# Kernel tuning notes

Measured on AMD Instinct MI355X. Metric: run time of the kernel, lower is better.

The kernel has to match this reference:

```python
import math
import jax, jax.numpy as jnp
import numpy as np

PHI = (1.0 + math.sqrt(5.0)) / 2.0
B, S, E, H, L = 2, 2048, 1024, 16, 5
DH = E // H


def setup_inputs() -> dict:
    key = jax.random.key(0)
    ks = jax.random.split(key, 16)
    rn = lambda k, sh, sc=0.02: jax.random.normal(k, sh, jnp.float32) * sc
    return {
        'x': jax.random.normal(ks[0], (B, S, E), jnp.float32),
        'consciousness_levels': jax.random.uniform(ks[1], (B, H), jnp.float32),
        'Wc': rn(ks[2], (L, E, E)), 'bc': jnp.zeros((L, E), jnp.float32),
        'Wf': rn(ks[3], (L, E, H)), 'bf': jnp.zeros((L, H), jnp.float32),
        'Wq': rn(ks[4], (E, E)), 'bq': jnp.zeros((E,), jnp.float32),
        'Wk': rn(ks[5], (E, E)), 'bk': jnp.zeros((E,), jnp.float32),
        'Wv': rn(ks[6], (E, E)), 'bv': jnp.zeros((E,), jnp.float32),
        'Wo': rn(ks[7], (E, E)), 'bo': jnp.zeros((E,), jnp.float32),
        'Wc1': rn(ks[8], (2 * DH, E)), 'bc1': jnp.zeros((E,), jnp.float32),
        'Wc2': rn(ks[9], (E, 1)), 'bc2': jnp.zeros((1,), jnp.float32),
        'gate': jax.random.normal(ks[10], (L, H), jnp.float32) / math.sqrt(H),
        'phi_phase': PHI * jnp.arange(H, dtype=jnp.float32),
        'ln_g': jnp.ones((E,), jnp.float32), 'ln_b': jnp.zeros((E,), jnp.float32),
    }


def reference(x, consciousness_levels, Wc, bc, Wf, bf, Wq, bq, Wk, bk, Wv, bv,
              Wo, bo, Wc1, bc1, Wc2, bc2, gate, phi_phase, ln_g, ln_b):
    b, s, e = x.shape
    l, _, h = Wf.shape
    dh = e // h
    # per-level consciousness scalar: consciousness_levels[:, level % num_heads] -> [B, L]
    cl = consciousness_levels[:, jnp.arange(l) % h]
    # consciousness-enhanced features: mean over L of (x @ Wc_l + bc_l) * cl[:, l]
    feat = jnp.einsum('bse,leo->lbso', x, Wc) + bc[:, None, None, :]   # [L,B,S,E]
    ce = jnp.mean(feat * cl.T[:, :, None, None], axis=0)                # [B,S,E]
    # QKV projections (spectral_norm linears; normalized weights supplied directly)
    Q = (ce @ Wq + bq).reshape(b, s, h, dh).transpose(0, 2, 1, 3)       # [B,H,S,Dh]
    K = (ce @ Wk + bk).reshape(b, s, h, dh).transpose(0, 2, 1, 3)
    V = (ce @ Wv + bv).reshape(b, s, h, dh).transpose(0, 2, 1, 3)
    scores = jnp.einsum('bhsd,bhtd->bhst', Q, K) / math.sqrt(dh)        # [B,H,S,S]
    # phi-harmonic phase modulation (scalar per (B,H), averaged over levels)
    pooled = ce.mean(axis=1)                                            # [B,E]
    freq = jnp.einsum('be,leh->lbh', pooled, Wf) + bf[:, None, :]       # [L,B,H]
    phase = jnp.sin(phi_phase[None, None, :] * freq * cl.T[:, :, None]).mean(axis=0)  # [B,H]
    scores = scores + 0.1 * phase[:, :, None, None]
    # quantum coherence gate per (B,H): sigmoid MLP on pooled Q/K head features
    ci = jnp.concatenate([Q.mean(axis=2), K.mean(axis=2)], axis=-1)     # [B,H,2*Dh]
    cw = jax.nn.sigmoid(jax.nn.gelu(ci @ Wc1 + bc1, approximate=False) @ Wc2 + bc2)  # [B,H,1]
    scores = scores * (1.0 + cw[..., None])
    aw = jax.nn.softmax(scores, axis=-1)
    # consciousness gating on attention weights, then re-softmax
    gw = jax.nn.softmax(gate, axis=1)                                   # [L,H]
    factor = jnp.prod(1.0 + 0.1 * cl[:, :, None] * gw[None, :, :], axis=1)  # [B,H]
    aw = jax.nn.softmax(aw * factor[:, :, None, None], axis=-1)
    attended = jnp.einsum('bhst,bhtd->bhsd', aw, V)
    out = attended.transpose(0, 2, 1, 3).reshape(b, s, e) @ Wo + bo
    y = x + out  # dropout is identity in eval
    mu = y.mean(axis=-1, keepdims=True)
    var = ((y - mu) ** 2).mean(axis=-1, keepdims=True)
    return (y - mu) / jnp.sqrt(var + 1e-5) * ln_g + ln_b
```

## Files before the change

### kernel.cpp

```cpp
#include <hip/hip_runtime.h>
#include <math.h>

#define BB 2
#define SS 2048
#define EE 1024
#define HH 16
#define LL 5
#define DH 64
#define QS (3 * EE)

typedef __attribute__((ext_vector_type(8))) short bf16x8;
typedef __attribute__((ext_vector_type(4))) float f32x4;

__device__ __forceinline__ unsigned short f2bf(float f) {
  unsigned u = __float_as_uint(f);
  u += 0x7fffu + ((u >> 16) & 1u);
  return (unsigned short)(u >> 16);
}
__device__ __forceinline__ float bf2f(unsigned short u) {
  return __uint_as_float((unsigned)u << 16);
}
__device__ __forceinline__ f32x4 mfma16(bf16x8 a, bf16x8 b, f32x4 c) {
  return __builtin_amdgcn_mfma_f32_16x16x32_bf16(a, b, c, 0, 0, 0);
}
__device__ __forceinline__ unsigned cvtpk(float a, float b) {
  unsigned r;
  asm("v_cvt_pk_bf16_f32 %0, %1, %2" : "=v"(r) : "v"(a), "v"(b));
  return r;
}
__device__ __forceinline__ void gload16(const unsigned short* g, unsigned short* l) {
  __builtin_amdgcn_global_load_lds(
      (const __attribute__((address_space(1))) void*)g,
      (__attribute__((address_space(3))) void*)l, 16, 0, 0);
}

__global__ void prep_kernel(const float* __restrict__ cons,
                            const float* __restrict__ gate,
                            float* __restrict__ cl, float* __restrict__ factor) {
  if (threadIdx.x == 0 && blockIdx.x == 0) {
    float clv[BB][LL];
    for (int b = 0; b < BB; ++b)
      for (int l = 0; l < LL; ++l) {
        clv[b][l] = cons[b * HH + (l % HH)];
        cl[b * LL + l] = clv[b][l];
      }
    float gw[LL][HH];
    for (int l = 0; l < LL; ++l) {
      float mx = -1e30f;
      for (int h = 0; h < HH; ++h) mx = fmaxf(mx, gate[l * HH + h]);
      float s = 0.f;
      for (int h = 0; h < HH; ++h) { gw[l][h] = expf(gate[l * HH + h] - mx); s += gw[l][h]; }
      for (int h = 0; h < HH; ++h) gw[l][h] /= s;
    }
    for (int b = 0; b < BB; ++b)
      for (int h = 0; h < HH; ++h) {
        float f = 1.f;
        for (int l = 0; l < LL; ++l) f *= 1.f + 0.1f * clv[b][l] * gw[l][h];
        factor[b * HH + h] = f;
      }
  }
}

__global__ void small_pack(const float* __restrict__ bc, const float* __restrict__ cl,
                           const float* __restrict__ bq, const float* __restrict__ bk,
                           const float* __restrict__ bv,
                           float* __restrict__ beff, float* __restrict__ bqkv) {
  int i = blockIdx.x * 256 + threadIdx.x;
  if (i < BB * EE) {
    int b = i >> 10, e = i & 1023;
    float a = 0.f;
    #pragma unroll
    for (int l = 0; l < LL; ++l) a += cl[b * LL + l] * bc[l * EE + e];
    beff[i] = a * (1.f / LL);
  } else {
    int j = i - BB * EE;
    float v = (j < EE) ? bq[j] : (j < 2 * EE) ? bk[j - EE] : bv[j - 2 * EE];
    bqkv[j] = v;
  }
}

__global__ __launch_bounds__(256) void wceffT_kernel(const float* __restrict__ Wc,
                                                     const float* __restrict__ cl,
                                                     unsigned short* __restrict__ Wt) {
  int o0 = blockIdx.x * 64, e0 = blockIdx.y * 64, b = blockIdx.z;
  __shared__ float t[64][69];
  int tid = threadIdx.x;
  float w[LL];
  #pragma unroll
  for (int l = 0; l < LL; ++l) w[l] = cl[b * LL + l] * (1.f / LL);
  #pragma unroll
  for (int i = 0; i < 4; ++i) {
    int idx = tid + i * 256;
    int r = idx >> 4, c4 = idx & 15;
    float4 acc = {0.f, 0.f, 0.f, 0.f};
    #pragma unroll
    for (int l = 0; l < LL; ++l) {
      float4 v = *(const float4*)&Wc[(long)l * EE * EE + (long)(e0 + r) * EE + o0 + c4 * 4];
      acc.x += w[l] * v.x; acc.y += w[l] * v.y; acc.z += w[l] * v.z; acc.w += w[l] * v.w;
    }
    t[r][c4 * 4 + 0] = acc.x; t[r][c4 * 4 + 1] = acc.y;
    t[r][c4 * 4 + 2] = acc.z; t[r][c4 * 4 + 3] = acc.w;
  }
  __syncthreads();
  #pragma unroll
  for (int i = 0; i < 2; ++i) {
    int idx = tid + i * 256;
    int o = idx >> 3, ech = idx & 7;
    unsigned short u[8];
    #pragma unroll
    for (int j = 0; j < 8; ++j) u[j] = f2bf(t[ech * 8 + j][o]);
    unsigned short* dst = Wt + (long)b * EE * EE + (long)(o0 + o) * EE + e0 + ech * 8;
    *(ushort4*)&dst[0] = *(ushort4*)&u[0];
    *(ushort4*)&dst[4] = *(ushort4*)&u[4];
  }
}

__global__ __launch_bounds__(256) void wT4_kernel(
    const float* __restrict__ W0, const float* __restrict__ W1,
    const float* __restrict__ W2, const float* __restrict__ W3,
    unsigned short* __restrict__ Wqkvt, unsigned short* __restrict__ Wot) {
  int z = blockIdx.z;
  const float* W = (z == 0) ? W0 : (z == 1) ? W1 : (z == 2) ? W2 : W3;
  unsigned short* Wt = (z < 3) ? (Wqkvt + (size_t)z * EE * EE) : Wot;
  int o0 = blockIdx.x * 64, e0 = blockIdx.y * 64;
  __shared__ float t[64][69];
  int tid = threadIdx.x;
  #pragma unroll
  for (int i = 0; i < 4; ++i) {
    int idx = tid + i * 256;
    int r = idx >> 4, c4 = idx & 15;
    float4 v = *(const float4*)&W[(long)(e0 + r) * EE + o0 + c4 * 4];
    t[r][c4 * 4 + 0] = v.x; t[r][c4 * 4 + 1] = v.y;
    t[r][c4 * 4 + 2] = v.z; t[r][c4 * 4 + 3] = v.w;
  }
  __syncthreads();
  #pragma unroll
  for (int i = 0; i < 2; ++i) {
    int idx = tid + i * 256;
    int o = idx >> 3, ech = idx & 7;
    unsigned short u[8];
    #pragma unroll
    for (int j = 0; j < 8; ++j) u[j] = f2bf(t[ech * 8 + j][o]);
    unsigned short* dst = Wt + (long)(o0 + o) * EE + e0 + ech * 8;
    *(ushort4*)&dst[0] = *(ushort4*)&u[0];
    *(ushort4*)&dst[4] = *(ushort4*)&u[4];
  }
}

__global__ void cvt_bf_kernel(const float* __restrict__ in, unsigned short* __restrict__ out) {
  long i = (long)blockIdx.x * 256 + threadIdx.x;
  float4 a = ((const float4*)in)[i * 2];
  float4 b = ((const float4*)in)[i * 2 + 1];
  ushort4 u0 = make_ushort4(f2bf(a.x), f2bf(a.y), f2bf(a.z), f2bf(a.w));
  ushort4 u1 = make_ushort4(f2bf(b.x), f2bf(b.y), f2bf(b.z), f2bf(b.w));
  ((ushort4*)out)[i * 2] = u0;
  ((ushort4*)out)[i * 2 + 1] = u1;
}

template <int OUTBF>
__global__ __launch_bounds__(256) void gemm_bf(
    const unsigned short* __restrict__ A, const unsigned short* __restrict__ Bt,
    const float* __restrict__ bias, void* __restrict__ C,
    int N, int K, long As_z, long Ws_z, long Bs_z, long Cs_z) {
  int flat = blockIdx.x + gridDim.x * (blockIdx.y + gridDim.y * blockIdx.z);
  int nwg = gridDim.x * gridDim.y * gridDim.z;
  flat = (flat & 7) * (nwg >> 3) + (flat >> 3);
  int nt_ = flat % gridDim.x;
  int rest = flat / gridDim.x;
  int mt_ = rest % gridDim.y;
  int z = rest / gridDim.y;

  const unsigned short* Ab = A + z * As_z + (long)mt_ * 128 * K;
  const unsigned short* Bb = Bt + z * Ws_z + (long)nt_ * 64 * K;
  const float* bb = bias + z * Bs_z + nt_ * 64;

  __shared__ __align__(16) unsigned short As[2][128 * 64];
  __shared__ __align__(16) unsigned short Bs[2][64 * 64];
  int tid = threadIdx.x;
  int w = tid >> 6, lane = tid & 63, c = lane & 15, g = lane >> 4;
  int wrow = (w >> 1) * 64, wcol = (w & 1) * 32;

  #define STAGE_A(kt, buf)                                                     \
    {                                                                          \
      const unsigned short* s_ = Ab + (kt) * 64;                               \
      _Pragma("unroll") for (int j = 0; j < 4; ++j) {                          \
        int base = (w * 4 + j) * 64;                                           \
        int idx = base + lane;                                                 \
        int row = idx >> 3, ch = idx & 7;                                      \
        gload16(s_ + (long)row * K + ((ch ^ (row & 7)) << 3),                  \
                &As[buf][base * 8]);                                           \
      }                                                                        \
    }
  #define STAGE_B(kt, buf)                                                     \
    {                                                                          \
      const unsigned short* s_ = Bb + (kt) * 64;                               \
      _Pragma("unroll") for (int j = 0; j < 2; ++j) {                          \
        int base = (w * 2 + j) * 64;                                           \
        int idx = base + lane;                                                 \
        int row = idx >> 3, ch = idx & 7;                                      \
        gload16(s_ + (long)row * K + ((ch ^ (row & 7)) << 3),                  \
                &Bs[buf][base * 8]);                                           \
      }                                                                        \
    }

  f32x4 acc[4][2];
  #pragma unroll
  for (int mi = 0; mi < 4; ++mi)
    #pragma unroll
    for (int ni = 0; ni < 2; ++ni) acc[mi][ni] = {0.f, 0.f, 0.f, 0.f};

  int nk = K >> 6;
  STAGE_A(0, 0) STAGE_B(0, 0)
  __syncthreads();
  int buf = 0;
  for (int kt = 0; kt < nk; ++kt) {
    if (kt + 1 < nk) { STAGE_A(kt + 1, buf ^ 1) STAGE_B(kt + 1, buf ^ 1) }
    #pragma unroll
    for (int kk = 0; kk < 2; ++kk) {
      bf16x8 af[4], bfv[2];
      #pragma unroll
      for (int mi = 0; mi < 4; ++mi) {
        int row = wrow + mi * 16 + c;
        af[mi] = *(const bf16x8*)&As[buf][row * 64 + ((((kk << 2) + g) ^ (row & 7)) << 3)];
      }
      #pragma unroll
      for (int ni = 0; ni < 2; ++ni) {
        int row = wcol + ni * 16 + c;
        bfv[ni] = *(const bf16x8*)&Bs[buf][row * 64 + ((((kk << 2) + g) ^ (row & 7)) << 3)];
      }
      #pragma unroll
      for (int mi = 0; mi < 4; ++mi)
        #pragma unroll
        for (int ni = 0; ni < 2; ++ni)
          acc[mi][ni] = mfma16(af[mi], bfv[ni], acc[mi][ni]);
    }
    __syncthreads();
    buf ^= 1;
  }

  float bval[2] = {bb[wcol + c], bb[wcol + 16 + c]};
  #pragma unroll
  for (int mi = 0; mi < 4; ++mi)
    #pragma unroll
    for (int ni = 0; ni < 2; ++ni) {
      long col = (long)nt_ * 64 + wcol + ni * 16 + c;
      #pragma unroll
      for (int r = 0; r < 4; ++r) {
        long row = (long)mt_ * 128 + wrow + mi * 16 + g * 4 + r;
        float v = acc[mi][ni][r] + bval[ni];
        if (OUTBF)
          ((unsigned short*)C)[z * Cs_z + row * N + col] = f2bf(v);
        else
          ((float*)C)[z * Cs_z + row * N + col] = v;
      }
    }
  #undef STAGE_A
  #undef STAGE_B
}

__global__ __launch_bounds__(256) void gemm128(
    const unsigned short* __restrict__ A, const unsigned short* __restrict__ Bt,
    const float* __restrict__ bias, unsigned short* __restrict__ C,
    int N, int K, long As_z, long Cs_z) {
  int flat = blockIdx.x + gridDim.x * (blockIdx.y + gridDim.y * blockIdx.z);
  int nwg = gridDim.x * gridDim.y * gridDim.z;
  flat = (flat & 7) * (nwg >> 3) + (flat >> 3);
  int nt_ = flat % gridDim.x;
  int rest = flat / gridDim.x;
  int mt_ = rest % gridDim.y;
  int z = rest / gridDim.y;

  const unsigned short* Ab = A + z * As_z + (long)mt_ * 128 * K;
  const unsigned short* Bb = Bt + (long)nt_ * 128 * K;
  const float* bb = bias + nt_ * 128;

  __shared__ __align__(16) unsigned short As[2][128 * 64];
  __shared__ __align__(16) unsigned short Bs[2][128 * 64];
  int tid = threadIdx.x;
  int w = tid >> 6, lane = tid & 63, c = lane & 15, g = lane >> 4;
  int wrow = (w >> 1) * 64, wcol = (w & 1) * 64;

  #define STG128(srcp, dstbuf, kt)                                             \
    {                                                                          \
      const unsigned short* s_ = (srcp) + (kt) * 64;                           \
      _Pragma("unroll") for (int j = 0; j < 4; ++j) {                          \
        int idx = tid + j * 256;                                               \
        int row = idx >> 3, ch = idx & 7;                                      \
        gload16(s_ + (long)row * K + ((ch ^ (row & 7)) << 3),                  \
                &dstbuf[(idx & ~63) * 8 + (lane)*8]);                          \
      }                                                                        \
    }

  f32x4 acc[4][4];
  #pragma unroll
  for (int mi = 0; mi < 4; ++mi)
    #pragma unroll
    for (int ni = 0; ni < 4; ++ni) acc[mi][ni] = {0.f, 0.f, 0.f, 0.f};

  int nk = K >> 6;
  STG128(Ab, As[0], 0) STG128(Bb, Bs[0], 0)
  __syncthreads();
  int buf = 0;
  for (int kt = 0; kt < nk; ++kt) {
    if (kt + 1 < nk) { STG128(Ab, As[buf ^ 1], kt + 1) STG128(Bb, Bs[buf ^ 1], kt + 1) }
    #pragma unroll
    for (int kk = 0; kk < 2; ++kk) {
      bf16x8 af[4], bfv[4];
      #pragma unroll
      for (int mi = 0; mi < 4; ++mi) {
        int row = wrow + mi * 16 + c;
        af[mi] = *(const bf16x8*)&As[buf][row * 64 + ((((kk << 2) + g) ^ (row & 7)) << 3)];
      }
      #pragma unroll
      for (int ni = 0; ni < 4; ++ni) {
        int row = wcol + ni * 16 + c;
        bfv[ni] = *(const bf16x8*)&Bs[buf][row * 64 + ((((kk << 2) + g) ^ (row & 7)) << 3)];
      }
      #pragma unroll
      for (int mi = 0; mi < 4; ++mi)
        #pragma unroll
        for (int ni = 0; ni < 4; ++ni)
          acc[mi][ni] = mfma16(af[mi], bfv[ni], acc[mi][ni]);
    }
    __syncthreads();
    buf ^= 1;
  }

  float bval[4];
  #pragma unroll
  for (int ni = 0; ni < 4; ++ni) bval[ni] = bb[wcol + ni * 16 + c];
  #pragma unroll
  for (int mi = 0; mi < 4; ++mi)
    #pragma unroll
    for (int ni = 0; ni < 4; ++ni) {
      long col = (long)nt_ * 128 + wcol + ni * 16 + c;
      #pragma unroll
      for (int r = 0; r < 4; ++r) {
        long row = (long)mt_ * 128 + wrow + mi * 16 + g * 4 + r;
        C[z * Cs_z + row * N + col] = f2bf(acc[mi][ni][r] + bval[ni]);
      }
    }
  #undef STG128
}

__global__ void mean2_kernel(const unsigned short* __restrict__ QKVb,
                             float* __restrict__ Qm, float* __restrict__ Km) {
  int z = blockIdx.z;
  const unsigned short* in = QKVb + z * EE;
  float* out = z ? Km : Qm;
  int e = blockIdx.x * 256 + threadIdx.x;
  int b = e >> 10, ee = e & 1023;
  int s0 = blockIdx.y * 128;
  const unsigned short* p = in + ((long)b * SS + s0) * QS + ee;
  float acc = 0.f;
  for (int i = 0; i < 128; ++i) acc += bf2f(p[(long)i * QS]);
  atomicAdd(&out[e], acc * (1.f / SS));
}

__global__ __launch_bounds__(256) void cw_kernel(
    const float* __restrict__ Qm, const float* __restrict__ Km,
    const float* __restrict__ Wc1, const float* __restrict__ bc1,
    const float* __restrict__ Wc2, const float* __restrict__ bc2,
    float* __restrict__ alpha) {
  int bh = blockIdx.x, b = bh / HH, h = bh % HH;
  __shared__ float ci[128];
  __shared__ float pr[4];
  int tid = threadIdx.x;
  if (tid < 64) ci[tid] = Qm[b * EE + h * DH + tid];
  else if (tid < 128) ci[tid] = Km[b * EE + h * DH + (tid - 64)];
  __syncthreads();
  float part = 0.f;
  for (int j = tid; j < EE; j += 256) {
    float acc = bc1[j];
    #pragma unroll 8
    for (int i = 0; i < 128; ++i) acc += ci[i] * Wc1[i * EE + j];
    float ge = 0.5f * acc * (1.f + erff(acc * 0.70710678118654752f));
    part += ge * Wc2[j];
  }
  #pragma unroll
  for (int off = 32; off; off >>= 1) part += __shfl_xor(part, off);
  if ((tid & 63) == 0) pr[tid >> 6] = part;
  __syncthreads();
  if (tid == 0) {
    float tot = pr[0] + pr[1] + pr[2] + pr[3] + bc2[0];
    float cw = 1.f / (1.f + expf(-tot));
    alpha[bh] = 1.f + cw;
  }
}

__global__ __launch_bounds__(256) void repack_vT(const unsigned short* __restrict__ Vh,
                                                 unsigned short* __restrict__ Vt) {
  int st = blockIdx.x, h = blockIdx.y, b = blockIdx.z;
  __shared__ unsigned short tile[64][66];
  int tid = threadIdx.x;
  const unsigned short* src = Vh + ((long)(b * SS) + st * 64) * QS + h * 64;
  #pragma unroll
  for (int i = 0; i < 2; ++i) {
    int idx = tid + i * 256;
    int s = idx >> 3, ch = idx & 7;
    #pragma unroll
    for (int j = 0; j < 8; ++j) tile[s][ch * 8 + j] = src[(long)s * QS + ch * 8 + j];
  }
  __syncthreads();
  unsigned short* dst = Vt + ((long)(b * HH + h) * 64) * SS + st * 64;
  #pragma unroll
  for (int i = 0; i < 2; ++i) {
    int idx = tid + i * 256;
    int d = idx >> 3, sch = idx & 7;
    unsigned short u[8];
    #pragma unroll
    for (int j = 0; j < 8; ++j) u[j] = tile[sch * 8 + j][d];
    *(ushort4*)&dst[(long)d * SS + sch * 8] = *(ushort4*)&u[0];
    *(ushort4*)&dst[(long)d * SS + sch * 8 + 4] = *(ushort4*)&u[4];
  }
}

__global__ __launch_bounds__(256) void vsum_kernel(const unsigned short* __restrict__ Vt,
                                                   float* __restrict__ Vsum) {
  int row = blockIdx.x * 4 + (threadIdx.x >> 6);
  int lane = threadIdx.x & 63;
  const unsigned short* p = Vt + (long)row * SS + lane * 32;
  float acc = 0.f;
  #pragma unroll
  for (int i = 0; i < 4; ++i) {
    uint4 v = *(const uint4*)(p + i * 8);
    unsigned arr[4] = {v.x, v.y, v.z, v.w};
    #pragma unroll
    for (int j = 0; j < 4; ++j) {
      acc += __uint_as_float(arr[j] << 16);
      acc += __uint_as_float(arr[j] & 0xffff0000u);
    }
  }
  #pragma unroll
  for (int off = 32; off; off >>= 1) acc += __shfl_xor(acc, off);
  if (lane == 0) Vsum[row] = acc;
}

__global__ __launch_bounds__(256, 4) void attn_lin(
    const unsigned short* __restrict__ QKV,
    const unsigned short* __restrict__ Vt,
    const float* __restrict__ alpha,
    float* __restrict__ Np0, float* __restrict__ Np1,
    float* __restrict__ m1p) {
  int flat = blockIdx.x;
  flat = (flat & 7) * 128 + (flat >> 3);
  int qt = flat & 15, h = (flat >> 4) & 15, b = (flat >> 8) & 1, part = flat >> 9;
  int bh = b * HH + h;
  int tid = threadIdx.x;
  int l = tid & 63, w = tid >> 6, c = l & 15, g = l >> 4;
  __shared__ __align__(16) unsigned short kbuf[4096];
  __shared__ __align__(16) unsigned short vbuf[4096];
  __shared__ __align__(16) unsigned short pws[4][1024];

  const unsigned short* Kb_ =
      QKV + (long)b * SS * QS + EE + h * 64 + (long)part * 1024 * QS;
  const unsigned short* Vb_ = Vt + (long)bh * 64 * SS + part * 1024;
  float* Np = part ? Np1 : Np0;
  const float scaleE = alpha[bh] * 0.125f;
  const f32x4 zero4 = {0.f, 0.f, 0.f, 0.f};

  bf16x8 qf[2][2];
  {
    const unsigned short* qp =
        QKV + ((long)b * SS + qt * 128 + w * 32 + c) * QS + h * 64;
    qf[0][0] = *(const bf16x8*)(qp + 8 * g);
    qf[0][1] = *(const bf16x8*)(qp + 32 + 8 * g);
    qf[1][0] = *(const bf16x8*)(qp + 16 * QS + 8 * g);
    qf[1][1] = *(const bf16x8*)(qp + 16 * QS + 32 + 8 * g);
  }

  int off1 = tid, off2 = tid + 256;
  int r1 = off1 >> 3, ch1 = ((off1 & 7) ^ (r1 & 7)) << 3;
  int r2 = off2 >> 3, ch2 = ((off2 & 7) ^ (r2 & 7)) << 3;
  const unsigned short* kg1 = Kb_ + (long)r1 * QS + ch1;
  const unsigned short* kg2 = Kb_ + (long)r2 * QS + ch2;
  const unsigned short* vg1 = Vb_ + (long)r1 * SS + ch1;
  const unsigned short* vg2 = Vb_ + (long)r2 * SS + ch2;

  uint4 ks1 = *(const uint4*)kg1, ks2 = *(const uint4*)kg2;
  uint4 vs1 = *(const uint4*)vg1, vs2 = *(const uint4*)vg2;
  kg1 += (long)64 * QS; kg2 += (long)64 * QS; vg1 += 64; vg2 += 64;
  *(uint4*)&kbuf[off1 * 8] = ks1; *(uint4*)&kbuf[off2 * 8] = ks2;
  *(uint4*)&vbuf[off1 * 8] = vs1; *(uint4*)&vbuf[off2 * 8] = vs2;
  __syncthreads();

  f32x4 N1[4][2];
  #pragma unroll
  for (int d = 0; d < 4; ++d) { N1[d][0] = zero4; N1[d][1] = zero4; }
  float m1l0 = 0.f, m1l1 = 0.f;
  unsigned short* pw = pws[w];

  const int NT2 = 16;
  for (int t = 0; t < NT2; ++t) {
    if (t + 1 < NT2) {
      ks1 = *(const uint4*)kg1; ks2 = *(const uint4*)kg2;
      vs1 = *(const uint4*)vg1; vs2 = *(const uint4*)vg2;
      kg1 += (long)64 * QS; kg2 += (long)64 * QS; vg1 += 64; vg2 += 64;
    }
    __builtin_amdgcn_s_setprio(1);
    #pragma unroll
    for (int half = 0; half < 2; ++half) {
      #pragma unroll
      for (int mth = 0; mth < 2; ++mth) {
        int mt = half * 2 + mth;
        int r = mt * 16 + c;
        bf16x8 a0 = *(const bf16x8*)&kbuf[r * 64 + ((g ^ (r & 7)) << 3)];
        bf16x8 a1 = *(const bf16x8*)&kbuf[r * 64 + (((4 + g) ^ (r & 7)) << 3)];
        int ch = 2 * mth + (g >> 1);
        #pragma unroll
        for (int qb = 0; qb < 2; ++qb) {
          f32x4 s = mfma16(a0, qf[qb][0], zero4);
          s = mfma16(a1, qf[qb][1], s);
          float u0 = __expf(s[0] * scaleE), u1 = __expf(s[1] * scaleE);
          float u2 = __expf(s[2] * scaleE), u3 = __expf(s[3] * scaleE);
          if (qb == 0) m1l0 += (u0 + u1) + (u2 + u3);
          else         m1l1 += (u0 + u1) + (u2 + u3);
          int row = qb * 16 + c;
          int swz = (ch ^ (row & 3) ^ ((row >> 2) & 3)) & 3;
          *(uint2*)&pw[row * 32 + (swz << 3) + ((g & 1) << 2)] =
              make_uint2(cvtpk(u0, u1), cvtpk(u2, u3));
        }
      }
      bf16x8 pf[2];
      #pragma unroll
      for (int qb = 0; qb < 2; ++qb) {
        int row = qb * 16 + c;
        int swz = (g ^ (row & 3) ^ ((row >> 2) & 3)) & 3;
        pf[qb] = *(const bf16x8*)&pw[row * 32 + (swz << 3)];
      }
      #pragma unroll
      for (int dblk = 0; dblk < 4; ++dblk) {
        int r = dblk * 16 + c;
        bf16x8 v = *(const bf16x8*)&vbuf[r * 64 + (((half * 4 + g) ^ (r & 7)) << 3)];
        N1[dblk][0] = mfma16(v, pf[0], N1[dblk][0]);
        N1[dblk][1] = mfma16(v, pf[1], N1[dblk][1]);
      }
    }
    __builtin_amdgcn_s_setprio(0);
    __syncthreads();
    if (t + 1 < NT2) {
      *(uint4*)&kbuf[off1 * 8] = ks1; *(uint4*)&kbuf[off2 * 8] = ks2;
      *(uint4*)&vbuf[off1 * 8] = vs1; *(uint4*)&vbuf[off2 * 8] = vs2;
    }
    __syncthreads();
  }

  m1l0 += __shfl_xor(m1l0, 16); m1l0 += __shfl_xor(m1l0, 32);
  m1l1 += __shfl_xor(m1l1, 16); m1l1 += __shfl_xor(m1l1, 32);
  if (l < 16) {
    long mb = ((long)(part * BB + b) * HH + h) * SS + qt * 128 + w * 32;
    m1p[mb + c] = m1l0;
    m1p[mb + 16 + c] = m1l1;
  }

  #pragma unroll
  for (int qb = 0; qb < 2; ++qb) {
    float* np = Np + ((long)b * SS + qt * 128 + w * 32 + qb * 16 + c) * EE + h * 64;
    #pragma unroll
    for (int dblk = 0; dblk < 4; ++dblk) {
      float4 o = {N1[dblk][qb][0], N1[dblk][qb][1], N1[dblk][qb][2], N1[dblk][qb][3]};
      *(float4*)&np[dblk * 16 + 4 * g] = o;
    }
  }
}

__global__ __launch_bounds__(256) void attn_combine(
    const float* __restrict__ Np0, const float* __restrict__ Np1,
    const float* __restrict__ m1p, const float* __restrict__ Vsum,
    const float* __restrict__ factor, unsigned short* __restrict__ att) {
  int row = blockIdx.x;
  int b = row >> 11, s = row & 2047;
  int e0 = threadIdx.x * 4;
  int h = e0 >> 6, d = e0 & 63;
  int bh = b * HH + h;
  float m1 = m1p[((long)b * HH + h) * SS + s] +
             m1p[((long)(BB + b) * HH + h) * SS + s];
  float fac = factor[bh];
  float c1 = fac / m1;
  float invden = 1.f / ((float)SS + fac);
  long base = (long)row * EE + e0;
  float4 n0 = *(const float4*)&Np0[base];
  float4 n1 = *(const float4*)&Np1[base];
  float4 vs = *(const float4*)&Vsum[bh * 64 + d];
  float o0 = (vs.x + c1 * (n0.x + n1.x)) * invden;
  float o1 = (vs.y + c1 * (n0.y + n1.y)) * invden;
  float o2 = (vs.z + c1 * (n0.z + n1.z)) * invden;
  float o3 = (vs.w + c1 * (n0.w + n1.w)) * invden;
  *(uint2*)&att[base] = make_uint2(cvtpk(o0, o1), cvtpk(o2, o3));
}

__global__ __launch_bounds__(256) void ln_kernel(
    const float* __restrict__ x, const float* __restrict__ proj,
    const float* __restrict__ g, const float* __restrict__ bb,
    float* __restrict__ out) {
  long row = blockIdx.x;
  const float* xp = x + row * EE;
  const float* pp = proj + row * EE;
  int tid = threadIdx.x;
  float v[4];
  float s = 0.f;
  __shared__ float r1[4], r2[4];
  #pragma unroll
  for (int i = 0; i < 4; ++i) {
    int e = tid + i * 256;
    v[i] = xp[e] + pp[e];
    s += v[i];
  }
  #pragma unroll
  for (int off = 32; off; off >>= 1) s += __shfl_xor(s, off);
  if ((tid & 63) == 0) r1[tid >> 6] = s;
  __syncthreads();
  float mean = (r1[0] + r1[1] + r1[2] + r1[3]) * (1.f / EE);
  float s2 = 0.f;
  #pragma unroll
  for (int i = 0; i < 4; ++i) { float d = v[i] - mean; s2 += d * d; }
  #pragma unroll
  for (int off = 32; off; off >>= 1) s2 += __shfl_xor(s2, off);
  if ((tid & 63) == 0) r2[tid >> 6] = s2;
  __syncthreads();
  float rstd = rsqrtf((r2[0] + r2[1] + r2[2] + r2[3]) * (1.f / EE) + 1e-5f);
  #pragma unroll
  for (int i = 0; i < 4; ++i) {
    int e = tid + i * 256;
    out[row * EE + e] = (v[i] - mean) * rstd * g[e] + bb[e];
  }
}

extern "C" void kernel_launch(void* const* d_in, const int* in_sizes, int n_in,
                              void* d_out, int out_size, void* d_ws, size_t ws_size,
                              hipStream_t stream) {
  (void)in_sizes; (void)n_in; (void)out_size; (void)ws_size;
  const float* x    = (const float*)d_in[0];
  const float* cons = (const float*)d_in[1];
  const float* Wc   = (const float*)d_in[2];
  const float* bc   = (const float*)d_in[3];
  const float* Wq   = (const float*)d_in[6];
  const float* bq   = (const float*)d_in[7];
  const float* Wk   = (const float*)d_in[8];
  const float* bk   = (const float*)d_in[9];
  const float* Wv   = (const float*)d_in[10];
  const float* bv   = (const float*)d_in[11];
  const float* Wo   = (const float*)d_in[12];
  const float* bo   = (const float*)d_in[13];
  const float* Wc1  = (const float*)d_in[14];
  const float* bc1  = (const float*)d_in[15];
  const float* Wc2  = (const float*)d_in[16];
  const float* bc2  = (const float*)d_in[17];
  const float* gate = (const float*)d_in[18];
  const float* ln_g = (const float*)d_in[20];
  const float* ln_b = (const float*)d_in[21];
  float* out = (float*)d_out;

  const size_t MSZ = (size_t)BB * SS * EE;
  float* p = (float*)d_ws;
  float* beff = p;  p += BB * EE;
  float* cl   = p;  p += 16;
  float* factor = p; p += 32;
  float* alpha  = p; p += 32;
  float* Qm   = p;  p += BB * EE;
  float* Km   = p;  p += BB * EE;
  float* bqkv = p;  p += QS;
  float* Vsum = p;  p += BB * EE;
  float* proj = p;  p += MSZ;
  unsigned short* q = (unsigned short*)p;
  unsigned short* xbf  = q;  q += MSZ;
  unsigned short* cebf = q;  q += MSZ;
  unsigned short* QKVb = q;  q += 3 * MSZ;
  unsigned short* Vt   = q;  q += MSZ;
  unsigned short* attb = q;  q += MSZ;
  unsigned short* Weft = q;  q += (size_t)BB * EE * EE;
  unsigned short* Wqkvt= q;  q += (size_t)3 * EE * EE;
  unsigned short* Wot  = q;  q += (size_t)EE * EE;
  float* m1p = (float*)q;    q += 2 * 2 * BB * HH * SS;
  float* Np0 = (float*)xbf;
  float* Np1 = proj;

  prep_kernel<<<1, 64, 0, stream>>>(cons, gate, cl, factor);
  small_pack<<<(BB * EE + QS) / 256, 256, 0, stream>>>(bc, cl, bq, bk, bv, beff, bqkv);
  wceffT_kernel<<<dim3(16, 16, 2), 256, 0, stream>>>(Wc, cl, Weft);
  wT4_kernel<<<dim3(16, 16, 4), 256, 0, stream>>>(Wq, Wk, Wv, Wo, Wqkvt, Wot);
  cvt_bf_kernel<<<MSZ / 8 / 256, 256, 0, stream>>>(x, xbf);

  dim3 ggrid(EE / 64, SS / 128, BB);
  gemm_bf<1><<<ggrid, 256, 0, stream>>>(xbf, Weft, beff, cebf, EE, EE,
                                        (long)SS * EE, (long)EE * EE, EE, (long)SS * EE);
  dim3 qgrid(QS / 128, SS / 128, BB);
  gemm128<<<qgrid, 256, 0, stream>>>(cebf, Wqkvt, bqkv, QKVb, QS, EE,
                                     (long)SS * EE, (long)SS * QS);

  hipMemsetAsync(Qm, 0, (size_t)2 * BB * EE * sizeof(float), stream);
  mean2_kernel<<<dim3((BB * EE) / 256, SS / 128, 2), 256, 0, stream>>>(QKVb, Qm, Km);
  cw_kernel<<<BB * HH, 256, 0, stream>>>(Qm, Km, Wc1, bc1, Wc2, bc2, alpha);

  repack_vT<<<dim3(SS / 64, HH, BB), 256, 0, stream>>>(QKVb + 2 * EE, Vt);
  vsum_kernel<<<(BB * EE) / 4, 256, 0, stream>>>(Vt, Vsum);

  attn_lin<<<1024, 256, 0, stream>>>(QKVb, Vt, alpha, Np0, Np1, m1p);
  attn_combine<<<BB * SS, 256, 0, stream>>>(Np0, Np1, m1p, Vsum, factor, attb);

  gemm_bf<0><<<ggrid, 256, 0, stream>>>(attb, Wot, bo, proj, EE, EE,
                                        (long)SS * EE, 0, 0, (long)SS * EE);
  ln_kernel<<<BB * SS, 256, 0, stream>>>(x, proj, ln_g, ln_b, out);
}
```

Baseline: 225.1 us.

## Split attention keys four ways with larger query tiles and bf16 partials

The attention kernel now covers 256 query rows per block (64 per wave) and splits the key dimension into four parts instead of two, so each K/V tile loaded into LDS is reused across more queries. The partial numerators are written as bf16 rather than fp32, and the combine kernel sums four partials. The prep and small_pack kernels are also merged into one launch that reads consciousness levels directly. This trades more registers (occupancy hint lowered from 4 to 3) and bf16 rounding of the partial sums for less global traffic and one fewer launch.

```diff
diff --git a/kernel.cpp b/kernel.cpp
--- a/kernel.cpp
+++ b/kernel.cpp
@@ -7,7 +7,7 @@
 #define HH 16
 #define LL 5
 #define DH 64
-#define QS (3 * EE)
+#define QS (3 * 1024)
 
 typedef __attribute__((ext_vector_type(8))) short bf16x8;
 typedef __attribute__((ext_vector_type(4))) float f32x4;
@@ -34,16 +34,14 @@
       (__attribute__((address_space(3))) void*)l, 16, 0, 0);
 }
 
-__global__ void prep_kernel(const float* __restrict__ cons,
-                            const float* __restrict__ gate,
-                            float* __restrict__ cl, float* __restrict__ factor) {
-  if (threadIdx.x == 0 && blockIdx.x == 0) {
-    float clv[BB][LL];
-    for (int b = 0; b < BB; ++b)
-      for (int l = 0; l < LL; ++l) {
-        clv[b][l] = cons[b * HH + (l % HH)];
-        cl[b * LL + l] = clv[b][l];
-      }
+__global__ void prep_pack(const float* __restrict__ cons, const float* __restrict__ gate,
+                          const float* __restrict__ bc,
+                          const float* __restrict__ bq, const float* __restrict__ bk,
+                          const float* __restrict__ bv,
+                          float* __restrict__ beff, float* __restrict__ bqkv,
+                          float* __restrict__ factor) {
+  int i = blockIdx.x * 256 + threadIdx.x;
+  if (i == 0) {
     float gw[LL][HH];
     for (int l = 0; l < LL; ++l) {
       float mx = -1e30f;
@@ -55,22 +53,15 @@
     for (int b = 0; b < BB; ++b)
       for (int h = 0; h < HH; ++h) {
         float f = 1.f;
-        for (int l = 0; l < LL; ++l) f *= 1.f + 0.1f * clv[b][l] * gw[l][h];
+        for (int l = 0; l < LL; ++l) f *= 1.f + 0.1f * cons[b * HH + l] * gw[l][h];
         factor[b * HH + h] = f;
       }
   }
-}
-
-__global__ void small_pack(const float* __restrict__ bc, const float* __restrict__ cl,
-                           const float* __restrict__ bq, const float* __restrict__ bk,
-                           const float* __restrict__ bv,
-                           float* __restrict__ beff, float* __restrict__ bqkv) {
-  int i = blockIdx.x * 256 + threadIdx.x;
   if (i < BB * EE) {
     int b = i >> 10, e = i & 1023;
     float a = 0.f;
     #pragma unroll
-    for (int l = 0; l < LL; ++l) a += cl[b * LL + l] * bc[l * EE + e];
+    for (int l = 0; l < LL; ++l) a += cons[b * HH + l] * bc[l * EE + e];
     beff[i] = a * (1.f / LL);
   } else {
     int j = i - BB * EE;
@@ -80,14 +71,14 @@
 }
 
 __global__ __launch_bounds__(256) void wceffT_kernel(const float* __restrict__ Wc,
-                                                     const float* __restrict__ cl,
+                                                     const float* __restrict__ cons,
                                                      unsigned short* __restrict__ Wt) {
   int o0 = blockIdx.x * 64, e0 = blockIdx.y * 64, b = blockIdx.z;
   __shared__ float t[64][69];
   int tid = threadIdx.x;
   float w[LL];
   #pragma unroll
-  for (int l = 0; l < LL; ++l) w[l] = cl[b * LL + l] * (1.f / LL);
+  for (int l = 0; l < LL; ++l) w[l] = cons[b * HH + l] * (1.f / LL);
   #pragma unroll
   for (int i = 0; i < 4; ++i) {
     int idx = tid + i * 256;
@@ -436,37 +427,39 @@
   if (lane == 0) Vsum[row] = acc;
 }
 
-__global__ __launch_bounds__(256, 4) void attn_lin(
+__global__ __launch_bounds__(256, 3) void attn_lin(
     const unsigned short* __restrict__ QKV,
     const unsigned short* __restrict__ Vt,
     const float* __restrict__ alpha,
-    float* __restrict__ Np0, float* __restrict__ Np1,
+    unsigned short* __restrict__ Np0, unsigned short* __restrict__ Np1,
+    unsigned short* __restrict__ Np2, unsigned short* __restrict__ Np3,
     float* __restrict__ m1p) {
   int flat = blockIdx.x;
   flat = (flat & 7) * 128 + (flat >> 3);
-  int qt = flat & 15, h = (flat >> 4) & 15, b = (flat >> 8) & 1, part = flat >> 9;
+  int qt = flat & 7, h = (flat >> 3) & 15, b = (flat >> 7) & 1, part = flat >> 8;
   int bh = b * HH + h;
   int tid = threadIdx.x;
   int l = tid & 63, w = tid >> 6, c = l & 15, g = l >> 4;
   __shared__ __align__(16) unsigned short kbuf[4096];
   __shared__ __align__(16) unsigned short vbuf[4096];
-  __shared__ __align__(16) unsigned short pws[4][1024];
+  __shared__ __align__(16) unsigned short pws[4][2048];
 
   const unsigned short* Kb_ =
-      QKV + (long)b * SS * QS + EE + h * 64 + (long)part * 1024 * QS;
-  const unsigned short* Vb_ = Vt + (long)bh * 64 * SS + part * 1024;
-  float* Np = part ? Np1 : Np0;
+      QKV + (long)b * SS * QS + EE + h * 64 + (long)part * 512 * QS;
+  const unsigned short* Vb_ = Vt + (long)bh * 64 * SS + part * 512;
+  unsigned short* Np = (part == 0) ? Np0 : (part == 1) ? Np1 : (part == 2) ? Np2 : Np3;
   const float scaleE = alpha[bh] * 0.125f;
   const f32x4 zero4 = {0.f, 0.f, 0.f, 0.f};
 
-  bf16x8 qf[2][2];
+  bf16x8 qf[4][2];
   {
     const unsigned short* qp =
-        QKV + ((long)b * SS + qt * 128 + w * 32 + c) * QS + h * 64;
-    qf[0][0] = *(const bf16x8*)(qp + 8 * g);
-    qf[0][1] = *(const bf16x8*)(qp + 32 + 8 * g);
-    qf[1][0] = *(const bf16x8*)(qp + 16 * QS + 8 * g);
-    qf[1][1] = *(const bf16x8*)(qp + 16 * QS + 32 + 8 * g);
+        QKV + ((long)b * SS + qt * 256 + w * 64 + c) * QS + h * 64;
+    #pragma unroll
+    for (int qb = 0; qb < 4; ++qb) {
+      qf[qb][0] = *(const bf16x8*)(qp + (long)qb * 16 * QS + 8 * g);
+      qf[qb][1] = *(const bf16x8*)(qp + (long)qb * 16 * QS + 32 + 8 * g);
+    }
   }
 
   int off1 = tid, off2 = tid + 256;
@@ -484,15 +477,17 @@
   *(uint4*)&vbuf[off1 * 8] = vs1; *(uint4*)&vbuf[off2 * 8] = vs2;
   __syncthreads();
 
-  f32x4 N1[4][2];
-  #pragma unroll
-  for (int d = 0; d < 4; ++d) { N1[d][0] = zero4; N1[d][1] = zero4; }
-  float m1l0 = 0.f, m1l1 = 0.f;
+  f32x4 N1[4][4];
+  #pragma unroll
+  for (int d = 0; d < 4; ++d)
+    #pragma unroll
+    for (int qq = 0; qq < 4; ++qq) N1[d][qq] = zero4;
+  float m1l0 = 0.f, m1l1 = 0.f, m1l2 = 0.f, m1l3 = 0.f;
   unsigned short* pw = pws[w];
 
-  const int NT2 = 16;
-  for (int t = 0; t < NT2; ++t) {
-    if (t + 1 < NT2) {
+  const int NT4 = 8;
+  for (int t = 0; t < NT4; ++t) {
+    if (t + 1 < NT4) {
       ks1 = *(const uint4*)kg1; ks2 = *(const uint4*)kg2;
       vs1 = *(const uint4*)vg1; vs2 = *(const uint4*)vg2;
       kg1 += (long)64 * QS; kg2 += (long)64 * QS; vg1 += 64; vg2 += 64;
@@ -508,37 +503,43 @@
         bf16x8 a1 = *(const bf16x8*)&kbuf[r * 64 + (((4 + g) ^ (r & 7)) << 3)];
         int ch = 2 * mth + (g >> 1);
         #pragma unroll
-        for (int qb = 0; qb < 2; ++qb) {
+        for (int qb = 0; qb < 4; ++qb) {
           f32x4 s = mfma16(a0, qf[qb][0], zero4);
           s = mfma16(a1, qf[qb][1], s);
           float u0 = __expf(s[0] * scaleE), u1 = __expf(s[1] * scaleE);
           float u2 = __expf(s[2] * scaleE), u3 = __expf(s[3] * scaleE);
-          if (qb == 0) m1l0 += (u0 + u1) + (u2 + u3);
-          else         m1l1 += (u0 + u1) + (u2 + u3);
+          float su = (u0 + u1) + (u2 + u3);
+          if (qb == 0) m1l0 += su;
+          else if (qb == 1) m1l1 += su;
+          else if (qb == 2) m1l2 += su;
+          else m1l3 += su;
           int row = qb * 16 + c;
           int swz = (ch ^ (row & 3) ^ ((row >> 2) & 3)) & 3;
           *(uint2*)&pw[row * 32 + (swz << 3) + ((g & 1) << 2)] =
               make_uint2(cvtpk(u0, u1), cvtpk(u2, u3));
         }
       }
-      bf16x8 pf[2];
-      #pragma unroll
-      for (int qb = 0; qb < 2; ++qb) {
-        int row = qb * 16 + c;
-        int swz = (g ^ (row & 3) ^ ((row >> 2) & 3)) & 3;
-        pf[qb] = *(const bf16x8*)&pw[row * 32 + (swz << 3)];
+      bf16x8 pf0, pf1, pf2, pf3;
+      {
+        int row0 = c, row1 = 16 + c, row2 = 32 + c, row3 = 48 + c;
+        pf0 = *(const bf16x8*)&pw[row0 * 32 + (((g ^ (row0 & 3) ^ ((row0 >> 2) & 3)) & 3) << 3)];
+        pf1 = *(const bf16x8*)&pw[row1 * 32 + (((g ^ (row1 & 3) ^ ((row1 >> 2) & 3)) & 3) << 3)];
+        pf2 = *(const bf16x8*)&pw[row2 * 32 + (((g ^ (row2 & 3) ^ ((row2 >> 2) & 3)) & 3) << 3)];
+        pf3 = *(const bf16x8*)&pw[row3 * 32 + (((g ^ (row3 & 3) ^ ((row3 >> 2) & 3)) & 3) << 3)];
       }
       #pragma unroll
       for (int dblk = 0; dblk < 4; ++dblk) {
         int r = dblk * 16 + c;
         bf16x8 v = *(const bf16x8*)&vbuf[r * 64 + (((half * 4 + g) ^ (r & 7)) << 3)];
-        N1[dblk][0] = mfma16(v, pf[0], N1[dblk][0]);
-        N1[dblk][1] = mfma16(v, pf[1], N1[dblk][1]);
+        N1[dblk][0] = mfma16(v, pf0, N1[dblk][0]);
+        N1[dblk][1] = mfma16(v, pf1, N1[dblk][1]);
+        N1[dblk][2] = mfma16(v, pf2, N1[dblk][2]);
+        N1[dblk][3] = mfma16(v, pf3, N1[dblk][3]);
       }
     }
     __builtin_amdgcn_s_setprio(0);
     __syncthreads();
-    if (t + 1 < NT2) {
+    if (t + 1 < NT4) {
       *(uint4*)&kbuf[off1 * 8] = ks1; *(uint4*)&kbuf[off2 * 8] = ks2;
       *(uint4*)&vbuf[off1 * 8] = vs1; *(uint4*)&vbuf[off2 * 8] = vs2;
     }
@@ -547,25 +548,32 @@
 
   m1l0 += __shfl_xor(m1l0, 16); m1l0 += __shfl_xor(m1l0, 32);
   m1l1 += __shfl_xor(m1l1, 16); m1l1 += __shfl_xor(m1l1, 32);
+  m1l2 += __shfl_xor(m1l2, 16); m1l2 += __shfl_xor(m1l2, 32);
+  m1l3 += __shfl_xor(m1l3, 16); m1l3 += __shfl_xor(m1l3, 32);
   if (l < 16) {
-    long mb = ((long)(part * BB + b) * HH + h) * SS + qt * 128 + w * 32;
+    long mb = ((long)(part * BB + b) * HH + h) * SS + qt * 256 + w * 64;
     m1p[mb + c] = m1l0;
     m1p[mb + 16 + c] = m1l1;
-  }
-
-  #pragma unroll
-  for (int qb = 0; qb < 2; ++qb) {
-    float* np = Np + ((long)b * SS + qt * 128 + w * 32 + qb * 16 + c) * EE + h * 64;
+    m1p[mb + 32 + c] = m1l2;
+    m1p[mb + 48 + c] = m1l3;
+  }
+
+  #pragma unroll
+  for (int qb = 0; qb < 4; ++qb) {
+    unsigned short* np =
+        Np + ((long)b * SS + qt * 256 + w * 64 + qb * 16 + c) * EE + h * 64;
     #pragma unroll
     for (int dblk = 0; dblk < 4; ++dblk) {
-      float4 o = {N1[dblk][qb][0], N1[dblk][qb][1], N1[dblk][qb][2], N1[dblk][qb][3]};
-      *(float4*)&np[dblk * 16 + 4 * g] = o;
+      *(uint2*)&np[dblk * 16 + 4 * g] =
+          make_uint2(cvtpk(N1[dblk][qb][0], N1[dblk][qb][1]),
+                     cvtpk(N1[dblk][qb][2], N1[dblk][qb][3]));
     }
   }
 }
 
 __global__ __launch_bounds__(256) void attn_combine(
-    const float* __restrict__ Np0, const float* __restrict__ Np1,
+    const unsigned short* __restrict__ Np0, const unsigned short* __restrict__ Np1,
+    const unsigned short* __restrict__ Np2, const unsigned short* __restrict__ Np3,
     const float* __restrict__ m1p, const float* __restrict__ Vsum,
     const float* __restrict__ factor, unsigned short* __restrict__ att) {
   int row = blockIdx.x;
@@ -573,19 +581,26 @@
   int e0 = threadIdx.x * 4;
   int h = e0 >> 6, d = e0 & 63;
   int bh = b * HH + h;
-  float m1 = m1p[((long)b * HH + h) * SS + s] +
-             m1p[((long)(BB + b) * HH + h) * SS + s];
+  long mi = ((long)b * HH + h) * SS + s;
+  const long mstep = (long)BB * HH * SS;
+  float m1 = m1p[mi] + m1p[mi + mstep] + m1p[mi + 2 * mstep] + m1p[mi + 3 * mstep];
   float fac = factor[bh];
   float c1 = fac / m1;
   float invden = 1.f / ((float)SS + fac);
   long base = (long)row * EE + e0;
-  float4 n0 = *(const float4*)&Np0[base];
-  float4 n1 = *(const float4*)&Np1[base];
+  ushort4 a0 = *(const ushort4*)&Np0[base];
+  ushort4 a1 = *(const ushort4*)&Np1[base];
+  ushort4 a2 = *(const ushort4*)&Np2[base];
+  ushort4 a3 = *(const ushort4*)&Np3[base];
   float4 vs = *(const float4*)&Vsum[bh * 64 + d];
-  float o0 = (vs.x + c1 * (n0.x + n1.x)) * invden;
-  float o1 = (vs.y + c1 * (n0.y + n1.y)) * invden;
-  float o2 = (vs.z + c1 * (n0.z + n1.z)) * invden;
-  float o3 = (vs.w + c1 * (n0.w + n1.w)) * invden;
+  float n0 = bf2f(a0.x) + bf2f(a1.x) + bf2f(a2.x) + bf2f(a3.x);
+  float n1 = bf2f(a0.y) + bf2f(a1.y) + bf2f(a2.y) + bf2f(a3.y);
+  float n2 = bf2f(a0.z) + bf2f(a1.z) + bf2f(a2.z) + bf2f(a3.z);
+  float n3 = bf2f(a0.w) + bf2f(a1.w) + bf2f(a2.w) + bf2f(a3.w);
+  float o0 = (vs.x + c1 * n0) * invden;
+  float o1 = (vs.y + c1 * n1) * invden;
+  float o2 = (vs.z + c1 * n2) * invden;
+  float o3 = (vs.w + c1 * n3) * invden;
   *(uint2*)&att[base] = make_uint2(cvtpk(o0, o1), cvtpk(o2, o3));
 }
 
@@ -654,7 +669,6 @@
   const size_t MSZ = (size_t)BB * SS * EE;
   float* p = (float*)d_ws;
   float* beff = p;  p += BB * EE;
-  float* cl   = p;  p += 16;
   float* factor = p; p += 32;
   float* alpha  = p; p += 32;
   float* Qm   = p;  p += BB * EE;
@@ -671,13 +685,15 @@
   unsigned short* Weft = q;  q += (size_t)BB * EE * EE;
   unsigned short* Wqkvt= q;  q += (size_t)3 * EE * EE;
   unsigned short* Wot  = q;  q += (size_t)EE * EE;
-  float* m1p = (float*)q;    q += 2 * 2 * BB * HH * SS;
-  float* Np0 = (float*)xbf;
-  float* Np1 = proj;
-
-  prep_kernel<<<1, 64, 0, stream>>>(cons, gate, cl, factor);
-  small_pack<<<(BB * EE + QS) / 256, 256, 0, stream>>>(bc, cl, bq, bk, bv, beff, bqkv);
-  wceffT_kernel<<<dim3(16, 16, 2), 256, 0, stream>>>(Wc, cl, Weft);
+  float* m1p = (float*)q;    q += 2 * 4 * BB * HH * SS;
+  unsigned short* Np0 = xbf;
+  unsigned short* Np1 = cebf;
+  unsigned short* Np2 = (unsigned short*)proj;
+  unsigned short* Np3 = (unsigned short*)proj + MSZ;
+
+  prep_pack<<<(BB * EE + QS) / 256, 256, 0, stream>>>(cons, gate, bc, bq, bk, bv,
+                                                      beff, bqkv, factor);
+  wceffT_kernel<<<dim3(16, 16, 2), 256, 0, stream>>>(Wc, cons, Weft);
   wT4_kernel<<<dim3(16, 16, 4), 256, 0, stream>>>(Wq, Wk, Wv, Wo, Wqkvt, Wot);
   cvt_bf_kernel<<<MSZ / 8 / 256, 256, 0, stream>>>(x, xbf);
 
@@ -695,8 +711,8 @@
   repack_vT<<<dim3(SS / 64, HH, BB), 256, 0, stream>>>(QKVb + 2 * EE, Vt);
   vsum_kernel<<<(BB * EE) / 4, 256, 0, stream>>>(Vt, Vsum);
 
-  attn_lin<<<1024, 256, 0, stream>>>(QKVb, Vt, alpha, Np0, Np1, m1p);
-  attn_combine<<<BB * SS, 256, 0, stream>>>(Np0, Np1, m1p, Vsum, factor, attb);
+  attn_lin<<<1024, 256, 0, stream>>>(QKVb, Vt, alpha, Np0, Np1, Np2, Np3, m1p);
+  attn_combine<<<BB * SS, 256, 0, stream>>>(Np0, Np1, Np2, Np3, m1p, Vsum, factor, attb);
 
   gemm_bf<0><<<ggrid, 256, 0, stream>>>(attb, Wot, bo, proj, EE, EE,
                                         (long)SS * EE, 0, 0, (long)SS * EE);
```

Result: slower. 267.2 us (+18.7%).
